# Kernel tuning notes

Hardware: AMD Instinct MI355X
Metric: run time of the kernel (lower is better)

## Reference

```python
import jax, jax.numpy as jnp
import numpy as np

B, N, A, H = 500000, 256, 64, 100  # batch, num_nodes, num_adj (edges at node), hidden width


def setup_inputs() -> dict:
    key = jax.random.key(0)
    ks = jax.random.split(key, 12)
    data = jax.random.normal(ks[0], (B, N), dtype=jnp.float32)
    weights = jax.random.normal(ks[1], (A,), dtype=jnp.float32)
    # edge buffers (constants registered in the torch module)
    data_idx = jax.random.randint(ks[2], (A,), 0, N)
    edge_directions = 2 * jax.random.randint(ks[3], (A,), 0, 2) - 1  # values in {-1, +1}
    weight_idx = jnp.arange(A)
    # MLP params: Linear(A,H), Linear(H,H), Linear(H,H), Linear(H,1) (torch default-ish init scale)
    def lin(k, fan_in, fan_out):
        s = 1.0 / np.sqrt(fan_in)
        kw, kb = jax.random.split(k)
        W = jax.random.uniform(kw, (fan_in, fan_out), jnp.float32, -s, s)
        b = jax.random.uniform(kb, (fan_out,), jnp.float32, -s, s)
        return W, b
    W1, b1 = lin(ks[4], A, H)
    W2, b2 = lin(ks[5], H, H)
    W3, b3 = lin(ks[6], H, H)
    W4, b4 = lin(ks[7], H, 1)
    return dict(data=data, weights=weights, W1=W1, b1=b1, W2=W2, b2=b2,
                W3=W3, b3=b3, W4=W4, b4=b4, data_idx=data_idx,
                edge_directions=edge_directions, weight_idx=weight_idx)


def reference(data, weights, W1, b1, W2, b2, W3, b3, W4, b4,
              data_idx, edge_directions, weight_idx):
    # per-edge gate: relu(weight * direction), shape [A]
    gate = jax.nn.relu(weights[weight_idx] * edge_directions.astype(weights.dtype))
    # fused gather over node columns + elementwise gate: [B, A]
    x = data[:, data_idx] * gate
    # stacked MLP: A -> H -> H -> H -> 1 with ReLU
    x = jax.nn.relu(x @ W1 + b1)
    x = jax.nn.relu(x @ W2 + b2)
    x = jax.nn.relu(x @ W3 + b3)
    return x @ W4 + b4  # [B, 1]
```

## Files before the change

kernel.cpp:

```cpp
#include <hip/hip_runtime.h>

#define BB 500000
#define NN 256
#define AA 64
#define HH 100

typedef short short8 __attribute__((ext_vector_type(8)));
typedef float float4v __attribute__((ext_vector_type(4)));

#define MFMA16(a, b, c) __builtin_amdgcn_mfma_f32_16x16x32_bf16((a), (b), (c), 0, 0, 0)

__device__ __forceinline__ short f2bf(float f) {
    unsigned u = __builtin_bit_cast(unsigned, f);
    u = (u + 0x7fffu + ((u >> 16) & 1u)) >> 16;
    return (short)u;
}

#define OFF_W1T   0
#define OFF_W2T   16128
#define OFF_W3T   46592
#define OFF_B1    77056
#define OFF_B2    77504
#define OFF_B3    77952
#define OFF_GATE  78400
#define OFF_X0    78656
#define OFF_X1    87872
#define OFF_X2    105280
#define LDS_TOTAL 122688

#define NTILES ((BB + 63) / 64)

__global__ void __launch_bounds__(256, 1)
nodal_mlp(const float* __restrict__ data, const float* __restrict__ weights,
          const float* __restrict__ W1, const float* __restrict__ b1,
          const float* __restrict__ W2, const float* __restrict__ b2,
          const float* __restrict__ W3, const float* __restrict__ b3,
          const float* __restrict__ W4, const float* __restrict__ b4,
          const int* __restrict__ didx, const int* __restrict__ edir,
          const int* __restrict__ widx, float* __restrict__ out)
{
    extern __shared__ char smem[];
    short* w1T  = (short*)(smem + OFF_W1T);
    short* w2T  = (short*)(smem + OFF_W2T);
    short* w3T  = (short*)(smem + OFF_W3T);
    float* b1p  = (float*)(smem + OFF_B1);
    float* b2p  = (float*)(smem + OFF_B2);
    float* b3p  = (float*)(smem + OFF_B3);
    float* gate = (float*)(smem + OFF_GATE);

    const int tid  = threadIdx.x;
    const int wave = tid >> 6;
    const int lane = tid & 63;
    const int m    = lane & 15;
    const int quad = lane >> 4;

    short* X0w = (short*)(smem + OFF_X0) + wave * (16 * 72);
    short* X1w = (short*)(smem + OFF_X1) + wave * (16 * 136);
    short* X2w = (short*)(smem + OFF_X2) + wave * (16 * 136);

    if (tid < AA)
        gate[tid] = fmaxf(weights[widx[tid]] * (float)edir[tid], 0.f);
    if (tid < 112) {
        b1p[tid] = (tid < HH) ? b1[tid] : 0.f;
        b2p[tid] = (tid < HH) ? b2[tid] : 0.f;
        b3p[tid] = (tid < HH) ? b3[tid] : 0.f;
    }
    for (int i = tid; i < 112 * 72; i += 256) w1T[i] = 0;
    for (int i = tid; i < 112 * 136; i += 256) { w2T[i] = 0; w3T[i] = 0; }
    for (int i = lane; i < 16 * 16; i += 64) {
        int r = i >> 4, k = 112 + (i & 15);
        X1w[r * 136 + k] = 0;
        X2w[r * 136 + k] = 0;
    }
    __syncthreads();
    for (int j = tid; j < AA * HH; j += 256) {
        int k = j / HH, n = j - k * HH;
        w1T[n * 72 + k] = f2bf(gate[k] * W1[j]);
    }
    for (int j = tid; j < HH * HH; j += 256) {
        int k = j / HH, n = j - k * HH;
        w2T[n * 136 + k] = f2bf(W2[j]);
        w3T[n * 136 + k] = f2bf(W3[j]);
    }
    __syncthreads();

    short8 w4f[4];
    #pragma unroll
    for (int ks = 0; ks < 4; ++ks) {
        #pragma unroll
        for (int j = 0; j < 8; ++j) {
            int k = ks * 32 + quad * 8 + j;
            w4f[ks][j] = (m == 0 && k < HH) ? f2bf(W4[k]) : (short)0;
        }
    }
    const float b4v   = b4[0];
    const int  colOff = didx[lane];

    float pf[16];
    int t = (int)blockIdx.x;
    {
        int r0 = t * 64 + wave * 16;
        const float* p = data + (size_t)colOff;
        if (r0 + 16 <= BB) {
            const float* q = p + (size_t)r0 * NN;
            #pragma unroll
            for (int r = 0; r < 16; ++r) pf[r] = q[r * NN];
        } else {
            #pragma unroll
            for (int r = 0; r < 16; ++r) {
                int row = r0 + r; row = row < BB ? row : BB - 1;
                pf[r] = p[(size_t)row * NN];
            }
        }
    }

    for (; t < NTILES; t += gridDim.x) {
        const int r0 = t * 64 + wave * 16;

        #pragma unroll
        for (int r = 0; r < 16; ++r)
            X0w[r * 72 + lane] = f2bf(pf[r]);

        int tn = t + (int)gridDim.x;
        if (tn < NTILES) {
            int r0n = tn * 64 + wave * 16;
            const float* p = data + (size_t)colOff;
            if (r0n + 16 <= BB) {
                const float* q = p + (size_t)r0n * NN;
                #pragma unroll
                for (int r = 0; r < 16; ++r) pf[r] = q[r * NN];
            } else {
                #pragma unroll
                for (int r = 0; r < 16; ++r) {
                    int row = r0n + r; row = row < BB ? row : BB - 1;
                    pf[r] = p[(size_t)row * NN];
                }
            }
        }

        {
            short8 a0 = *(const short8*)(X0w + m * 72 + quad * 8);
            short8 a1 = *(const short8*)(X0w + m * 72 + 32 + quad * 8);
            #pragma unroll
            for (int nt = 0; nt < 7; ++nt) {
                const short* wp = w1T + (nt * 16 + m) * 72 + quad * 8;
                float4v c = {0.f, 0.f, 0.f, 0.f};
                c = MFMA16(a0, *(const short8*)(wp), c);
                c = MFMA16(a1, *(const short8*)(wp + 32), c);
                float bias = b1p[nt * 16 + m];
                #pragma unroll
                for (int i = 0; i < 4; ++i)
                    X1w[(quad * 4 + i) * 136 + nt * 16 + m] =
                        f2bf(fmaxf(c[i] + bias, 0.f));
            }
        }

        #pragma unroll
        for (int L = 0; L < 2; ++L) {
            const short* Xin  = L ? X2w : X1w;
            short*       Xout = L ? X1w : X2w;
            const short* wT   = L ? w3T : w2T;
            const float* bp   = L ? b3p : b2p;
            short8 a[4];
            #pragma unroll
            for (int ks = 0; ks < 4; ++ks)
                a[ks] = *(const short8*)(Xin + m * 136 + ks * 32 + quad * 8);
            #pragma unroll
            for (int nt = 0; nt < 7; ++nt) {
                float4v c = {0.f, 0.f, 0.f, 0.f};
                #pragma unroll
                for (int ks = 0; ks < 4; ++ks)
                    c = MFMA16(a[ks],
                               *(const short8*)(wT + (nt * 16 + m) * 136 + ks * 32 + quad * 8),
                               c);
                float bias = bp[nt * 16 + m];
                #pragma unroll
                for (int i = 0; i < 4; ++i)
                    Xout[(quad * 4 + i) * 136 + nt * 16 + m] =
                        f2bf(fmaxf(c[i] + bias, 0.f));
            }
        }

        {
            float4v c = {0.f, 0.f, 0.f, 0.f};
            #pragma unroll
            for (int ks = 0; ks < 4; ++ks) {
                short8 a = *(const short8*)(X1w + m * 136 + ks * 32 + quad * 8);
                c = MFMA16(a, w4f[ks], c);
            }
            if (m == 0) {
                #pragma unroll
                for (int i = 0; i < 4; ++i) {
                    int row = r0 + quad * 4 + i;
                    if (row < BB) out[row] = c[i] + b4v;
                }
            }
        }
    }
}

extern "C" void kernel_launch(void* const* d_in, const int* in_sizes, int n_in,
                              void* d_out, int out_size, void* d_ws, size_t ws_size,
                              hipStream_t stream) {
    (void)in_sizes; (void)n_in; (void)d_ws; (void)ws_size; (void)out_size;
    const float* data    = (const float*)d_in[0];
    const float* weights = (const float*)d_in[1];
    const float* W1      = (const float*)d_in[2];
    const float* b1      = (const float*)d_in[3];
    const float* W2      = (const float*)d_in[4];
    const float* b2      = (const float*)d_in[5];
    const float* W3      = (const float*)d_in[6];
    const float* b3      = (const float*)d_in[7];
    const float* W4      = (const float*)d_in[8];
    const float* b4      = (const float*)d_in[9];
    const int*   didx    = (const int*)d_in[10];
    const int*   edir    = (const int*)d_in[11];
    const int*   widx    = (const int*)d_in[12];
    float* out = (float*)d_out;

    hipFuncSetAttribute((const void*)nodal_mlp,
                        hipFuncAttributeMaxDynamicSharedMemorySize, LDS_TOTAL);
    nodal_mlp<<<256, 256, LDS_TOTAL, stream>>>(
        data, weights, W1, b1, W2, b2, W3, b3, W4, b4, didx, edir, widx, out);
}
```

Before: 711.7 us.

## Double rows per wave, reuse weight fragments across two subtiles, run 8 waves

Measured after the change: 697.4 us. 1.02x faster.

```diff
diff --git a/kernel.cpp b/kernel.cpp
--- a/kernel.cpp
+++ b/kernel.cpp
@@ -23,14 +23,13 @@
 #define OFF_B2    77504
 #define OFF_B3    77952
 #define OFF_GATE  78400
-#define OFF_X0    78656
-#define OFF_X1    87872
-#define OFF_X2    105280
-#define LDS_TOTAL 122688
-
-#define NTILES ((BB + 63) / 64)
-
-__global__ void __launch_bounds__(256, 1)
+#define OFF_X     78656
+#define LDS_TOTAL 148288
+
+#define ROWS_PER_TILE 256
+#define NTILES ((BB + ROWS_PER_TILE - 1) / ROWS_PER_TILE)
+
+__global__ void __launch_bounds__(512, 2)
 nodal_mlp(const float* __restrict__ data, const float* __restrict__ weights,
           const float* __restrict__ W1, const float* __restrict__ b1,
           const float* __restrict__ W2, const float* __restrict__ b2,
@@ -54,9 +53,7 @@
     const int m    = lane & 15;
     const int quad = lane >> 4;
 
-    short* X0w = (short*)(smem + OFF_X0) + wave * (16 * 72);
-    short* X1w = (short*)(smem + OFF_X1) + wave * (16 * 136);
-    short* X2w = (short*)(smem + OFF_X2) + wave * (16 * 136);
+    short* Xw = (short*)(smem + OFF_X) + wave * (32 * 136);
 
     if (tid < AA)
         gate[tid] = fmaxf(weights[widx[tid]] * (float)edir[tid], 0.f);
@@ -65,19 +62,18 @@
         b2p[tid] = (tid < HH) ? b2[tid] : 0.f;
         b3p[tid] = (tid < HH) ? b3[tid] : 0.f;
     }
-    for (int i = tid; i < 112 * 72; i += 256) w1T[i] = 0;
-    for (int i = tid; i < 112 * 136; i += 256) { w2T[i] = 0; w3T[i] = 0; }
-    for (int i = lane; i < 16 * 16; i += 64) {
+    for (int i = tid; i < 112 * 72; i += 512) w1T[i] = 0;
+    for (int i = tid; i < 112 * 136; i += 512) { w2T[i] = 0; w3T[i] = 0; }
+    for (int i = lane; i < 32 * 16; i += 64) {
         int r = i >> 4, k = 112 + (i & 15);
-        X1w[r * 136 + k] = 0;
-        X2w[r * 136 + k] = 0;
+        Xw[r * 136 + k] = 0;
     }
     __syncthreads();
-    for (int j = tid; j < AA * HH; j += 256) {
+    for (int j = tid; j < AA * HH; j += 512) {
         int k = j / HH, n = j - k * HH;
         w1T[n * 72 + k] = f2bf(gate[k] * W1[j]);
     }
-    for (int j = tid; j < HH * HH; j += 256) {
+    for (int j = tid; j < HH * HH; j += 512) {
         int k = j / HH, n = j - k * HH;
         w2T[n * 136 + k] = f2bf(W2[j]);
         w3T[n * 136 + k] = f2bf(W3[j]);
@@ -96,18 +92,18 @@
     const float b4v   = b4[0];
     const int  colOff = didx[lane];
 
-    float pf[16];
+    float pf[32];
     int t = (int)blockIdx.x;
     {
-        int r0 = t * 64 + wave * 16;
+        int r0 = t * ROWS_PER_TILE + wave * 32;
         const float* p = data + (size_t)colOff;
-        if (r0 + 16 <= BB) {
+        if (r0 + 32 <= BB) {
             const float* q = p + (size_t)r0 * NN;
             #pragma unroll
-            for (int r = 0; r < 16; ++r) pf[r] = q[r * NN];
+            for (int r = 0; r < 32; ++r) pf[r] = q[r * NN];
         } else {
             #pragma unroll
-            for (int r = 0; r < 16; ++r) {
+            for (int r = 0; r < 32; ++r) {
                 int row = r0 + r; row = row < BB ? row : BB - 1;
                 pf[r] = p[(size_t)row * NN];
             }
@@ -115,83 +111,101 @@
     }
 
     for (; t < NTILES; t += gridDim.x) {
-        const int r0 = t * 64 + wave * 16;
-
-        #pragma unroll
-        for (int r = 0; r < 16; ++r)
-            X0w[r * 72 + lane] = f2bf(pf[r]);
-
-        int tn = t + (int)gridDim.x;
-        if (tn < NTILES) {
-            int r0n = tn * 64 + wave * 16;
-            const float* p = data + (size_t)colOff;
-            if (r0n + 16 <= BB) {
-                const float* q = p + (size_t)r0n * NN;
-                #pragma unroll
-                for (int r = 0; r < 16; ++r) pf[r] = q[r * NN];
-            } else {
-                #pragma unroll
-                for (int r = 0; r < 16; ++r) {
-                    int row = r0n + r; row = row < BB ? row : BB - 1;
-                    pf[r] = p[(size_t)row * NN];
-                }
-            }
-        }
+        const int r0 = t * ROWS_PER_TILE + wave * 32;
+
+        #pragma unroll
+        for (int r = 0; r < 32; ++r)
+            Xw[r * 136 + lane] = f2bf(pf[r]);
 
         {
-            short8 a0 = *(const short8*)(X0w + m * 72 + quad * 8);
-            short8 a1 = *(const short8*)(X0w + m * 72 + 32 + quad * 8);
+            int tn = t + (int)gridDim.x;
+            if (tn < NTILES) {
+                int r0n = tn * ROWS_PER_TILE + wave * 32;
+                const float* p = data + (size_t)colOff;
+                if (r0n + 32 <= BB) {
+                    const float* q = p + (size_t)r0n * NN;
+                    #pragma unroll
+                    for (int r = 0; r < 32; ++r) pf[r] = q[r * NN];
+                } else {
+                    #pragma unroll
+                    for (int r = 0; r < 32; ++r) {
+                        int row = r0n + r; row = row < BB ? row : BB - 1;
+                        pf[r] = p[(size_t)row * NN];
+                    }
+                }
+            }
+        }
+
+        {
+            short8 a1[2][2];
+            #pragma unroll
+            for (int sub = 0; sub < 2; ++sub)
+                #pragma unroll
+                for (int ks = 0; ks < 2; ++ks)
+                    a1[sub][ks] = *(const short8*)(Xw + (sub * 16 + m) * 136 + ks * 32 + quad * 8);
             #pragma unroll
             for (int nt = 0; nt < 7; ++nt) {
                 const short* wp = w1T + (nt * 16 + m) * 72 + quad * 8;
-                float4v c = {0.f, 0.f, 0.f, 0.f};
-                c = MFMA16(a0, *(const short8*)(wp), c);
-                c = MFMA16(a1, *(const short8*)(wp + 32), c);
+                short8 w0 = *(const short8*)(wp);
+                short8 w1v = *(const short8*)(wp + 32);
                 float bias = b1p[nt * 16 + m];
                 #pragma unroll
-                for (int i = 0; i < 4; ++i)
-                    X1w[(quad * 4 + i) * 136 + nt * 16 + m] =
-                        f2bf(fmaxf(c[i] + bias, 0.f));
+                for (int sub = 0; sub < 2; ++sub) {
+                    float4v c = {0.f, 0.f, 0.f, 0.f};
+                    c = MFMA16(a1[sub][0], w0, c);
+                    c = MFMA16(a1[sub][1], w1v, c);
+                    #pragma unroll
+                    for (int i = 0; i < 4; ++i)
+                        Xw[(sub * 16 + quad * 4 + i) * 136 + nt * 16 + m] =
+                            f2bf(fmaxf(c[i] + bias, 0.f));
+                }
             }
         }
 
         #pragma unroll
         for (int L = 0; L < 2; ++L) {
-            const short* Xin  = L ? X2w : X1w;
-            short*       Xout = L ? X1w : X2w;
-            const short* wT   = L ? w3T : w2T;
-            const float* bp   = L ? b3p : b2p;
-            short8 a[4];
-            #pragma unroll
-            for (int ks = 0; ks < 4; ++ks)
-                a[ks] = *(const short8*)(Xin + m * 136 + ks * 32 + quad * 8);
+            const short* wT = L ? w3T : w2T;
+            const float* bp = L ? b3p : b2p;
+            short8 a[2][4];
+            #pragma unroll
+            for (int sub = 0; sub < 2; ++sub)
+                #pragma unroll
+                for (int ks = 0; ks < 4; ++ks)
+                    a[sub][ks] = *(const short8*)(Xw + (sub * 16 + m) * 136 + ks * 32 + quad * 8);
             #pragma unroll
             for (int nt = 0; nt < 7; ++nt) {
-                float4v c = {0.f, 0.f, 0.f, 0.f};
+                const short* wp = wT + (nt * 16 + m) * 136 + quad * 8;
+                short8 wf[4];
                 #pragma unroll
                 for (int ks = 0; ks < 4; ++ks)
-                    c = MFMA16(a[ks],
-                               *(const short8*)(wT + (nt * 16 + m) * 136 + ks * 32 + quad * 8),
-                               c);
+                    wf[ks] = *(const short8*)(wp + ks * 32);
                 float bias = bp[nt * 16 + m];
                 #pragma unroll
-                for (int i = 0; i < 4; ++i)
-                    Xout[(quad * 4 + i) * 136 + nt * 16 + m] =
-                        f2bf(fmaxf(c[i] + bias, 0.f));
-            }
-        }
-
-        {
+                for (int sub = 0; sub < 2; ++sub) {
+                    float4v c = {0.f, 0.f, 0.f, 0.f};
+                    #pragma unroll
+                    for (int ks = 0; ks < 4; ++ks)
+                        c = MFMA16(a[sub][ks], wf[ks], c);
+                    #pragma unroll
+                    for (int i = 0; i < 4; ++i)
+                        Xw[(sub * 16 + quad * 4 + i) * 136 + nt * 16 + m] =
+                            f2bf(fmaxf(c[i] + bias, 0.f));
+                }
+            }
+        }
+
+        #pragma unroll
+        for (int sub = 0; sub < 2; ++sub) {
             float4v c = {0.f, 0.f, 0.f, 0.f};
             #pragma unroll
             for (int ks = 0; ks < 4; ++ks) {
-                short8 a = *(const short8*)(X1w + m * 136 + ks * 32 + quad * 8);
+                short8 a = *(const short8*)(Xw + (sub * 16 + m) * 136 + ks * 32 + quad * 8);
                 c = MFMA16(a, w4f[ks], c);
             }
             if (m == 0) {
                 #pragma unroll
                 for (int i = 0; i < 4; ++i) {
-                    int row = r0 + quad * 4 + i;
+                    int row = r0 + sub * 16 + quad * 4 + i;
                     if (row < BB) out[row] = c[i] + b4v;
                 }
             }
@@ -220,6 +234,6 @@
 
     hipFuncSetAttribute((const void*)nodal_mlp,
                         hipFuncAttributeMaxDynamicSharedMemorySize, LDS_TOTAL);
-    nodal_mlp<<<256, 256, LDS_TOTAL, stream>>>(
+    nodal_mlp<<<256, 512, LDS_TOTAL, stream>>>(
         data, weights, W1, b1, W2, b2, W3, b3, W4, b4, didx, edir, widx, out);
 }
```
